# Kernel tuning notes

Measured on AMD Instinct MI355X. Metric: run time of the kernel, lower is better.

The kernel has to match this reference:

```python
import jax, jax.numpy as jnp
import numpy as np

SMPL_PARENTS = [-1, 0, 0, 0, 1, 2, 3, 4, 5, 6, 7, 8, 9, 9, 9, 12, 13, 14, 16, 17, 18, 19, 20, 21]
J = 24          # SMPL_NR_JOINTS
HID = 32        # hidden_dim
LSTM_H = HID * J  # 768

# Static skeleton adjacency incl. self loops (PyG GATConv add_self_loops=True).
# Edge (parent v -> child u): messages flow src=v to dst=u. adj[dst, src] = True.
_adj = np.eye(J, dtype=bool)
for u, v in enumerate(SMPL_PARENTS):
    if v >= 0:
        _adj[u, v] = True
ADJ = jnp.asarray(_adj)


def setup_inputs() -> dict:
    key = jax.random.key(0)
    ks = jax.random.split(key, 12)
    N, L = 128, 256
    s = lambda k, shp, scale: (jax.random.normal(k, shp, dtype=jnp.float32) * scale)
    return {
        "src": s(ks[0], (N, L, J * 3), 1.0),
        # pre: Linear(3 -> 32) + tanh
        "W_pre": s(ks[1], (3, HID), 0.3),
        "b_pre": s(ks[2], (HID,), 0.05),
        # GATConv(32 -> 32, heads=1): lin (no bias), att_src, att_dst, out bias
        "W_gat": s(ks[3], (HID, HID), 0.15),
        "att_src": s(ks[4], (HID,), 0.15),
        "att_dst": s(ks[5], (HID,), 0.15),
        "b_gat": s(ks[6], (HID,), 0.05),
        # LSTM(768 -> 768), gate order i, f, g, o (torch convention)
        "W_ih": s(ks[7], (4 * LSTM_H, LSTM_H), 0.02),
        "W_hh": s(ks[8], (4 * LSTM_H, LSTM_H), 0.02),
        "b_ih": s(ks[9], (4 * LSTM_H,), 0.02),
        "b_hh": s(ks[10], (4 * LSTM_H,), 0.02),
    }


def _gat_lstm(src, W_pre, b_pre, W_gat, att_src, att_dst, b_gat, W_ih, W_hh, b_ih, b_hh):
    N, L, D = src.shape
    A = D // J
    x = src.reshape(N * L, J, A)                       # [B, J, 3]
    x = jnp.tanh(x @ W_pre + b_pre)                    # pre: [B, J, H]

    # GATConv (heads=1, concat): vectorized over B copies of the static skeleton.
    xp = x @ W_gat                                     # [B, J, H]
    a_s = xp @ att_src                                 # [B, J] source term
    a_d = xp @ att_dst                                 # [B, J] dest term
    # e[b, i, j] = LeakyReLU(a_d[i] + a_s[j]) for edge j -> i (incl. self loops)
    e = jax.nn.leaky_relu(a_d[:, :, None] + a_s[:, None, :], negative_slope=0.2)
    e = jnp.where(ADJ[None, :, :], e, -jnp.inf)
    attn = jax.nn.softmax(e, axis=-1)                  # softmax over incoming edges
    g = jnp.einsum('bij,bjh->bih', attn, xp) + b_gat   # [B, J, H]

    X = g.reshape(N, L, J * HID)                       # from_graph_seq -> [N, L, 768]

    # LSTM (num_layers=1, batch_first), torch gate order i, f, g, o
    def step(carry, x_t):
        h, c = carry
        gates = x_t @ W_ih.T + b_ih + h @ W_hh.T + b_hh  # [N, 4*768]
        i_g, f_g, g_g, o_g = jnp.split(gates, 4, axis=-1)
        c = jax.nn.sigmoid(f_g) * c + jax.nn.sigmoid(i_g) * jnp.tanh(g_g)
        h = jax.nn.sigmoid(o_g) * jnp.tanh(c)
        return (h, c), h

    h0 = jnp.zeros((N, LSTM_H), dtype=X.dtype)
    (h_n, c_n), ys = jax.lax.scan(step, (h0, h0), X.transpose(1, 0, 2))
    output = ys.transpose(1, 0, 2)                     # [N, L, 768]
    return output, h_n[None], c_n[None]                # (out, (h_n, c_n)) like nn.LSTM


def reference(src, W_pre, b_pre, W_gat, att_src, att_dst, b_gat, W_ih, W_hh, b_ih, b_hh):
    return _gat_lstm(src, W_pre, b_pre, W_gat, att_src, att_dst, b_gat, W_ih, W_hh, b_ih, b_hh)
```

## Files before the change

### kernel.cpp

```cpp
#include <hip/hip_runtime.h>
#include <hip/hip_bf16.h>


#define NB 128
#define LSEQ 256
#define LH 768
#define BGR 32768
#define NWG 96
#define PWG 192

typedef __attribute__((ext_vector_type(8))) short short8;
typedef __attribute__((ext_vector_type(4))) float floatx4;
typedef __attribute__((ext_vector_type(4))) unsigned int uint4v;
typedef __attribute__((ext_vector_type(2))) unsigned int uint2v;

union frag16 { uint4v u; short8 s; };
union bfbits { __hip_bfloat16 h; unsigned short s; };
union uf2 { uint2v u; float f[2]; };

__device__ __forceinline__ float fsig(float x) {
    return __builtin_amdgcn_rcpf(1.f + __builtin_amdgcn_exp2f(-1.44269504f * x));
}
__device__ __forceinline__ float ftanhf(float x) {
    return 1.f - 2.f * __builtin_amdgcn_rcpf(1.f + __builtin_amdgcn_exp2f(2.88539008f * x));
}
__device__ __forceinline__ float fexpf(float x) {
    return __builtin_amdgcn_exp2f(1.44269504f * x);
}

__device__ __forceinline__ float bf16bits_to_f(unsigned short s) {
    unsigned u = ((unsigned)s) << 16;
    float f;
    __builtin_memcpy(&f, &u, 4);
    return f;
}

__device__ __forceinline__ void issue8(uint4v* b, const char* base) {
    asm volatile("global_load_dwordx4 %0, %1, off sc0 sc1"            : "=v"(b[0]) : "v"(base));
    asm volatile("global_load_dwordx4 %0, %1, off offset:64 sc0 sc1"  : "=v"(b[1]) : "v"(base));
    asm volatile("global_load_dwordx4 %0, %1, off offset:128 sc0 sc1" : "=v"(b[2]) : "v"(base));
    asm volatile("global_load_dwordx4 %0, %1, off offset:192 sc0 sc1" : "=v"(b[3]) : "v"(base));
    asm volatile("global_load_dwordx4 %0, %1, off offset:256 sc0 sc1" : "=v"(b[4]) : "v"(base));
    asm volatile("global_load_dwordx4 %0, %1, off offset:320 sc0 sc1" : "=v"(b[5]) : "v"(base));
    asm volatile("global_load_dwordx4 %0, %1, off offset:384 sc0 sc1" : "=v"(b[6]) : "v"(base));
    asm volatile("global_load_dwordx4 %0, %1, off offset:448 sc0 sc1" : "=v"(b[7]) : "v"(base));
}
__device__ __forceinline__ void issueG2(uint2v* g, const char* gb) {
    const char* gb2 = gb + 6144;
    asm volatile("global_load_dwordx2 %0, %1, off"             : "=v"(g[0]) : "v"(gb));
    asm volatile("global_load_dwordx2 %0, %1, off offset:3072" : "=v"(g[1]) : "v"(gb));
    asm volatile("global_load_dwordx2 %0, %1, off"             : "=v"(g[2]) : "v"(gb2));
    asm volatile("global_load_dwordx2 %0, %1, off offset:3072" : "=v"(g[3]) : "v"(gb2));
}
__device__ __forceinline__ void wait16g_touch(uint4v* b, uint2v* g) {
    asm volatile("s_waitcnt vmcnt(16)"
        : "+v"(b[0]), "+v"(b[1]), "+v"(b[2]), "+v"(b[3]),
          "+v"(b[4]), "+v"(b[5]), "+v"(b[6]), "+v"(b[7]),
          "+v"(g[0]), "+v"(g[1]), "+v"(g[2]), "+v"(g[3]) :: "memory");
}
__device__ __forceinline__ void wait8_touch(uint4v* b) {
    asm volatile("s_waitcnt vmcnt(8)"
        : "+v"(b[0]), "+v"(b[1]), "+v"(b[2]), "+v"(b[3]),
          "+v"(b[4]), "+v"(b[5]), "+v"(b[6]), "+v"(b[7]) :: "memory");
}
__device__ __forceinline__ void wait0_touch(uint4v* b) {
    asm volatile("s_waitcnt vmcnt(0)"
        : "+v"(b[0]), "+v"(b[1]), "+v"(b[2]), "+v"(b[3]),
          "+v"(b[4]), "+v"(b[5]), "+v"(b[6]), "+v"(b[7]) :: "memory");
}

__global__ __launch_bounds__(256) void convert_kernel(
    const float* W_pre, const float* b_pre, const float* W_gat,
    const float* att_src, const float* att_dst, const float* b_gat,
    const float* W_ih, const float* W_hh, const float* b_ih, const float* b_hh,
    __hip_bfloat16* __restrict__ WihC, __hip_bfloat16* __restrict__ WhhC,
    float* __restrict__ smallC)
{
    long i = (long)blockIdx.x * 256 + threadIdx.x;
    if (i < 2359296) { WihC[i] = __float2bfloat16(W_ih[i]); return; }
    i -= 2359296;
    if (i < 2359296) { WhhC[i] = __float2bfloat16(W_hh[i]); return; }
    i -= 2359296;
    if (i < 96)   { smallC[0 + i]    = W_pre[i];   return; }  i -= 96;
    if (i < 32)   { smallC[96 + i]   = b_pre[i];   return; }  i -= 32;
    if (i < 1024) { smallC[128 + i]  = W_gat[i];   return; }  i -= 1024;
    if (i < 32)   { smallC[1152 + i] = att_src[i]; return; }  i -= 32;
    if (i < 32)   { smallC[1184 + i] = att_dst[i]; return; }  i -= 32;
    if (i < 32)   { smallC[1216 + i] = b_gat[i];   return; }  i -= 32;
    if (i < 3072) { smallC[1248 + i] = b_ih[i];    return; }  i -= 3072;
    if (i < 3072) { smallC[4320 + i] = b_hh[i];    return; }
}

__global__ __launch_bounds__(256) void gat_pre_kernel(
    const float* __restrict__ src,
    const float* __restrict__ smallC,
    __hip_bfloat16* __restrict__ Xb)
{
    __shared__ float wpre[96];
    __shared__ float bpre[32];
    __shared__ float wgat[1024];
    __shared__ float asrc[32];
    __shared__ float adst[32];
    __shared__ float bgat[32];
    __shared__ float xl[8][72];
    __shared__ float hl[8][24][32];
    __shared__ float xpl[8][24][32];
    __shared__ float asl[8][24];
    __shared__ float adl[8][24];

    const int tid = threadIdx.x;
    for (int i = tid; i < 96; i += 256)   wpre[i] = smallC[i];
    for (int i = tid; i < 1024; i += 256) wgat[i] = smallC[128 + i];
    if (tid < 32) {
        bpre[tid] = smallC[96 + tid];
        asrc[tid] = smallC[1152 + tid];
        adst[tid] = smallC[1184 + tid];
        bgat[tid] = smallC[1216 + tid];
    }

    const int g = tid >> 5;
    const int k = tid & 31;
    const long gb = (long)blockIdx.x * 8 + g;

    for (int i = k; i < 72; i += 32)
        xl[g][i] = src[gb * 72 + i];
    __syncthreads();

    #pragma unroll
    for (int j = 0; j < 24; ++j) {
        float v = xl[g][j*3+0] * wpre[0*32+k]
                + xl[g][j*3+1] * wpre[1*32+k]
                + xl[g][j*3+2] * wpre[2*32+k] + bpre[k];
        hl[g][j][k] = ftanhf(v);
    }
    __syncthreads();

    #pragma unroll
    for (int j = 0; j < 24; ++j) {
        float v = 0.f;
        #pragma unroll
        for (int m = 0; m < 32; ++m) v += hl[g][j][m] * wgat[m*32 + k];
        xpl[g][j][k] = v;
    }
    __syncthreads();

    if (k < 24) {
        float vs = 0.f, vd = 0.f;
        #pragma unroll
        for (int m = 0; m < 32; ++m) {
            float x = xpl[g][k][m];
            vs += x * asrc[m];
            vd += x * adst[m];
        }
        asl[g][k] = vs;
        adl[g][k] = vd;
    }
    __syncthreads();

    const int par[24] = {-1,0,0,0,1,2,3,4,5,6,7,8,9,9,9,12,13,14,16,17,18,19,20,21};
    #pragma unroll
    for (int j = 0; j < 24; ++j) {
        int p = par[j];
        float o;
        if (p < 0) {
            o = xpl[g][j][k] + bgat[k];
        } else {
            float es = adl[g][j] + asl[g][j];
            float ep = adl[g][j] + asl[g][p];
            es = es > 0.f ? es : 0.2f * es;
            ep = ep > 0.f ? ep : 0.2f * ep;
            float mx = fmaxf(es, ep);
            float wse = fexpf(es - mx), wpe = fexpf(ep - mx);
            float inv = __builtin_amdgcn_rcpf(wse + wpe);
            o = (wse * xpl[g][j][k] + wpe * xpl[g][p][k]) * inv + bgat[k];
        }
        Xb[gb * 768 + j * 32 + k] = __float2bfloat16(o);
    }
}

__global__ __launch_bounds__(256) void gates_in_kernel(
    const __hip_bfloat16* __restrict__ Xb,
    const __hip_bfloat16* __restrict__ Wih,
    const float* __restrict__ smallC,
    float* __restrict__ Gf, __hip_bfloat16* __restrict__ Gb, int ginf)
{
    const int tid = threadIdx.x;
    const int w = tid >> 6, L = tid & 63;
    const int rh2 = w >> 1, ch2 = w & 1;
    const int q = L >> 4, col16 = L & 15;
    const int bid = blockIdx.x;
    const int g2 = bid >> 10;
    const int r2 = bid & 1023;
    const int R0 = (r2 >> 2) * 128;
    const int N0 = ((g2 << 2) | (r2 & 3)) * 128;

    const short8* ap[4];
    const short8* bp[4];
    #pragma unroll
    for (int i = 0; i < 4; ++i) {
        ap[i] = (const short8*)(Xb + (size_t)(R0 + 64*rh2 + 16*i + col16) * 768 + q*8);
        bp[i] = (const short8*)(Wih + (size_t)(N0 + 64*ch2 + 16*i + col16) * 768 + q*8);
    }

    floatx4 acc[4][4] = {};
    for (int kk = 0; kk < 24; ++kk) {
        short8 a[4], b[4];
        #pragma unroll
        for (int i = 0; i < 4; ++i) { a[i] = ap[i][kk*4]; b[i] = bp[i][kk*4]; }
        #pragma unroll
        for (int rt = 0; rt < 4; ++rt)
            #pragma unroll
            for (int bt = 0; bt < 4; ++bt)
                acc[rt][bt] = __builtin_amdgcn_mfma_f32_16x16x32_bf16(a[rt], b[bt], acc[rt][bt], 0, 0, 0);
    }

    #pragma unroll
    for (int bt = 0; bt < 4; ++bt) {
        int wrow = N0 + 64*ch2 + 16*bt + col16;
        float bias = smallC[1248 + wrow] + smallC[4320 + wrow];
        #pragma unroll
        for (int rt = 0; rt < 4; ++rt) {
            #pragma unroll
            for (int r = 0; r < 4; ++r) {
                int m_abs = R0 + 64*rh2 + 16*rt + q*4 + r;
                int mm = m_abs >> 8, tt = m_abs & 255;
                size_t idx = ((size_t)tt * 128 + mm) * 3072 + wrow;
                float v = acc[rt][bt][r] + bias;
                if (ginf) Gf[idx] = v;
                else      Gb[idx] = __float2bfloat16(v);
            }
        }
    }
}

__global__ __launch_bounds__(256) void lstm_persist_kernel(
    const void* __restrict__ Gin,
    const __hip_bfloat16* __restrict__ Whh,
    __hip_bfloat16* __restrict__ h0g,
    __hip_bfloat16* __restrict__ h1g,
    float* __restrict__ out,
    int* __restrict__ barU,
    int ginf)
{
    __shared__ short8 whhs[3072];
    __shared__ float gl[64 * 33];

    const int tid = threadIdx.x;
    const int w = tid >> 6;
    const int L = tid & 63;
    const int q = L >> 4;
    const int col16 = L & 15;
    const int cg = blockIdx.x % 96;
    const int rg = blockIdx.x / 96;

    for (int b = 0; b < 12; ++b) {
        int f = tid + 256 * b;
        int kk = f >> 7, c = (f >> 2) & 31, qq = f & 3;
        int wrow = 768 * (c >> 3) + cg * 8 + (c & 7);
        whhs[f] = *(const short8*)(Whh + (size_t)wrow * 768 + kk * 32 + qq * 8);
    }
    __syncthreads();

    const int m_loc = tid >> 2;
    const int u2b = (tid & 3) * 2;
    const int m_glob = rg * 64 + m_loc;
    float creg0 = 0.f, creg1 = 0.f;

    const float* Gf = (const float*)Gin;
    const __hip_bfloat16* Gb = (const __hip_bfloat16*)Gin;
    const size_t gcol = cg * 8 + u2b;

    int* myL1    = &barU[(rg * 16 + (cg & 7)) * 32];
    int* myL2    = &barU[(rg * 16 + 8) * 32];
    int* myEpoch = &barU[(rg * 16 + 9) * 32];

    uint2v gp[4] = {};
    if (ginf)
        issueG2(gp, (const char*)(Gf + (size_t)m_glob * 3072 + gcol));

    for (int t = 0; t < LSEQ; ++t) {
        const char* hr = (const char*)((t & 1) ? h1g : h0g);
        __hip_bfloat16* hw = (t & 1) ? h0g : h1g;

        floatx4 acc0 = {}, acc1 = {};
        uint4v bufA[8], bufB[8], bufC[8];
        const char* hbase = hr + (size_t)(((rg * 64 + 16 * w + col16) * 768) + q * 8) * 2;

        issue8(bufA, hbase);
        issue8(bufB, hbase + 512);
        issue8(bufC, hbase + 1024);

        wait16g_touch(bufA, gp);
        #pragma unroll
        for (int j = 0; j < 8; ++j) {
            frag16 fu; fu.u = bufA[j];
            short8 bv0 = whhs[j * 128 + (col16 * 4 + q)];
            short8 bv1 = whhs[j * 128 + ((16 + col16) * 4 + q)];
            acc0 = __builtin_amdgcn_mfma_f32_16x16x32_bf16(fu.s, bv0, acc0, 0, 0, 0);
            acc1 = __builtin_amdgcn_mfma_f32_16x16x32_bf16(fu.s, bv1, acc1, 0, 0, 0);
        }
        wait8_touch(bufB);
        #pragma unroll
        for (int j = 0; j < 8; ++j) {
            frag16 fu; fu.u = bufB[j];
            short8 bv0 = whhs[(8 + j) * 128 + (col16 * 4 + q)];
            short8 bv1 = whhs[(8 + j) * 128 + ((16 + col16) * 4 + q)];
            acc0 = __builtin_amdgcn_mfma_f32_16x16x32_bf16(fu.s, bv0, acc0, 0, 0, 0);
            acc1 = __builtin_amdgcn_mfma_f32_16x16x32_bf16(fu.s, bv1, acc1, 0, 0, 0);
        }
        wait0_touch(bufC);
        #pragma unroll
        for (int j = 0; j < 8; ++j) {
            frag16 fu; fu.u = bufC[j];
            short8 bv0 = whhs[(16 + j) * 128 + (col16 * 4 + q)];
            short8 bv1 = whhs[(16 + j) * 128 + ((16 + col16) * 4 + q)];
            acc0 = __builtin_amdgcn_mfma_f32_16x16x32_bf16(fu.s, bv0, acc0, 0, 0, 0);
            acc1 = __builtin_amdgcn_mfma_f32_16x16x32_bf16(fu.s, bv1, acc1, 0, 0, 0);
        }

        #pragma unroll
        for (int r = 0; r < 4; ++r) {
            int mr = 16 * w + q * 4 + r;
            gl[mr * 33 + col16] = acc0[r];
            gl[mr * 33 + 16 + col16] = acc1[r];
        }
        __syncthreads();

        float gI0, gI1, gF0, gF1, gG0, gG1, gO0, gO1;
        if (ginf) {
            uf2 uI, uF, uG, uO;
            uI.u = gp[0]; uF.u = gp[1]; uG.u = gp[2]; uO.u = gp[3];
            gI0 = uI.f[0]; gI1 = uI.f[1]; gF0 = uF.f[0]; gF1 = uF.f[1];
            gG0 = uG.f[0]; gG1 = uG.f[1]; gO0 = uO.f[0]; gO1 = uO.f[1];
        } else {
            const size_t grow = ((size_t)t * 128 + m_glob) * 3072 + gcol;
            unsigned vi = *(const unsigned*)(Gb + grow);
            unsigned vf = *(const unsigned*)(Gb + grow + 768);
            unsigned vg = *(const unsigned*)(Gb + grow + 1536);
            unsigned vo = *(const unsigned*)(Gb + grow + 2304);
            gI0 = bf16bits_to_f(vi & 0xFFFF); gI1 = bf16bits_to_f(vi >> 16);
            gF0 = bf16bits_to_f(vf & 0xFFFF); gF1 = bf16bits_to_f(vf >> 16);
            gG0 = bf16bits_to_f(vg & 0xFFFF); gG1 = bf16bits_to_f(vg >> 16);
            gO0 = bf16bits_to_f(vo & 0xFFFF); gO1 = bf16bits_to_f(vo >> 16);
        }

        float ig0 = gI0 + gl[m_loc * 33 + 0  + u2b];
        float fg0 = gF0 + gl[m_loc * 33 + 8  + u2b];
        float gg0 = gG0 + gl[m_loc * 33 + 16 + u2b];
        float og0 = gO0 + gl[m_loc * 33 + 24 + u2b];
        float ig1 = gI1 + gl[m_loc * 33 + 0  + u2b + 1];
        float fg1 = gF1 + gl[m_loc * 33 + 8  + u2b + 1];
        float gg1 = gG1 + gl[m_loc * 33 + 16 + u2b + 1];
        float og1 = gO1 + gl[m_loc * 33 + 24 + u2b + 1];

        float si0 = fsig(ig0), sf0 = fsig(fg0), so0 = fsig(og0);
        float cn0 = sf0 * creg0 + si0 * ftanhf(gg0);
        float hv0 = so0 * ftanhf(cn0);
        creg0 = cn0;
        float si1 = fsig(ig1), sf1 = fsig(fg1), so1 = fsig(og1);
        float cn1 = sf1 * creg1 + si1 * ftanhf(gg1);
        float hv1 = so1 * ftanhf(cn1);
        creg1 = cn1;

        bfbits b0, b1;
        b0.h = __float2bfloat16(hv0);
        b1.h = __float2bfloat16(hv1);
        unsigned hpack = (unsigned)b0.s | ((unsigned)b1.s << 16);
        char* ha = (char*)hw + (size_t)(m_glob * 768 + cg * 8 + u2b) * 2;
        float2 ov; ov.x = hv0; ov.y = hv1;
        float* oa = out + ((size_t)m_glob * 256 + t) * 768 + cg * 8 + u2b;

        if (t < LSEQ - 1) {
            asm volatile("global_store_dword %0, %1, off sc0 sc1" :: "v"(ha), "v"(hpack) : "memory");
            asm volatile("global_store_dwordx2 %0, %1, off" :: "v"(oa), "v"(ov) : "memory");
            if (ginf)
                issueG2(gp, (const char*)(Gf + ((size_t)(t + 1) * 128 + m_glob) * 3072 + gcol));
            asm volatile("s_waitcnt vmcnt(5)" ::: "memory");
            __builtin_amdgcn_s_barrier();
            if (tid == 0) {
                int prev = __hip_atomic_fetch_add(myL1, 1,
                                                  __ATOMIC_RELAXED, __HIP_MEMORY_SCOPE_AGENT);
                bool rel = false;
                if (prev == 12 * (t + 1) - 1) {
                    int pr = __hip_atomic_fetch_add(myL2, 1,
                                                    __ATOMIC_RELAXED, __HIP_MEMORY_SCOPE_AGENT);
                    if (pr == 8 * (t + 1) - 1) {
                        __hip_atomic_store(myEpoch, t + 1,
                                           __ATOMIC_RELAXED, __HIP_MEMORY_SCOPE_AGENT);
                        rel = true;
                    }
                }
                if (!rel) {
                    while (__hip_atomic_load(myEpoch, __ATOMIC_RELAXED,
                                             __HIP_MEMORY_SCOPE_AGENT) < t + 1)
                        __builtin_amdgcn_s_sleep(1);
                }
            }
            __builtin_amdgcn_s_barrier();
        } else {
            asm volatile("global_store_dwordx2 %0, %1, off" :: "v"(oa), "v"(ov) : "memory");
            const size_t base = (size_t)NB * LSEQ * LH;
            const size_t ci = (size_t)m_glob * 768 + cg * 8 + u2b;
            float2 hv; hv.x = hv0; hv.y = hv1;
            float2 cv; cv.x = cn0; cv.y = cn1;
            *(float2*)(out + base + ci) = hv;
            *(float2*)(out + base + (size_t)NB * LH + ci) = cv;
        }
    }
}

__global__ __launch_bounds__(256) void lstm_step_kernel(
    const __hip_bfloat16* __restrict__ Xb,
    const __hip_bfloat16* __restrict__ Wih,
    const __hip_bfloat16* __restrict__ Whh,
    const float* __restrict__ smallC,
    float* __restrict__ cst,
    const __hip_bfloat16* __restrict__ hr,
    __hip_bfloat16* __restrict__ hw,
    float* __restrict__ out,
    int t)
{
    __shared__ float gls[128 * 33];
    const int tid = threadIdx.x;
    const int w = tid >> 6;
    const int L = tid & 63;
    const int rh = w >> 1;
    const int ct = w & 1;
    const int q = L >> 4;
    const int col16 = L & 15;
    const int c_local = 16 * ct + col16;
    const int gate = c_local >> 3;
    const int uu = c_local & 7;
    const int u = 8 * blockIdx.x + uu;
    const int wrow = 768 * gate + u;

    const short8* bp_i = (const short8*)(Wih + (long)wrow * 768 + q * 8);
    const short8* bp_h = (const short8*)(Whh + (long)wrow * 768 + q * 8);
    const short8* ap_x[4];
    const short8* ap_h[4];
    #pragma unroll
    for (int rt = 0; rt < 4; ++rt) {
        int m = 64 * rh + 16 * rt + col16;
        ap_x[rt] = (const short8*)(Xb + ((long)m * LSEQ + t) * 768 + q * 8);
        ap_h[rt] = (const short8*)(hr + (long)m * 768 + q * 8);
    }
    floatx4 acc[4] = {};
    for (int kk = 0; kk < 768; kk += 32) {
        short8 bv = bp_i[kk >> 3];
        #pragma unroll
        for (int rt = 0; rt < 4; ++rt)
            acc[rt] = __builtin_amdgcn_mfma_f32_16x16x32_bf16(ap_x[rt][kk >> 3], bv, acc[rt], 0, 0, 0);
    }
    for (int kk = 0; kk < 768; kk += 32) {
        short8 bv = bp_h[kk >> 3];
        #pragma unroll
        for (int rt = 0; rt < 4; ++rt)
            acc[rt] = __builtin_amdgcn_mfma_f32_16x16x32_bf16(ap_h[rt][kk >> 3], bv, acc[rt], 0, 0, 0);
    }
    float bias = smallC[1248 + wrow] + smallC[4320 + wrow];
    #pragma unroll
    for (int rt = 0; rt < 4; ++rt)
        #pragma unroll
        for (int r = 0; r < 4; ++r) {
            int m = 64 * rh + 16 * rt + q * 4 + r;
            gls[m * 33 + c_local] = acc[rt][r] + bias;
        }
    __syncthreads();
    for (int item = tid; item < 1024; item += 256) {
        int m = item >> 3;
        int u2l = item & 7;
        float ig = gls[m * 33 + 0  + u2l];
        float fg = gls[m * 33 + 8  + u2l];
        float gg = gls[m * 33 + 16 + u2l];
        float og = gls[m * 33 + 24 + u2l];
        int u2 = 8 * blockIdx.x + u2l;
        int ci = m * 768 + u2;
        float co = cst[ci];
        float si = 1.f / (1.f + expf(-ig));
        float sf = 1.f / (1.f + expf(-fg));
        float so = 1.f / (1.f + expf(-og));
        float cn = sf * co + si * tanhf(gg);
        float h = so * tanhf(cn);
        cst[ci] = cn;
        hw[ci] = __float2bfloat16(h);
        out[((long)m * LSEQ + t) * 768 + u2] = h;
    }
}

__global__ __launch_bounds__(256) void finalize_kernel(
    const __hip_bfloat16* __restrict__ hfin,
    const float* __restrict__ cst,
    float* __restrict__ out)
{
    int i = blockIdx.x * 256 + threadIdx.x;
    const long base = (long)NB * LSEQ * LH;
    out[base + i] = __bfloat162float(hfin[i]);
    out[base + NB * LH + i] = cst[i];
}

extern "C" void kernel_launch(void* const* d_in, const int* in_sizes, int n_in,
                              void* d_out, int out_size, void* d_ws, size_t ws_size,
                              hipStream_t stream) {
    const float* src     = (const float*)d_in[0];
    const float* W_pre   = (const float*)d_in[1];
    const float* b_pre   = (const float*)d_in[2];
    const float* W_gat   = (const float*)d_in[3];
    const float* att_src = (const float*)d_in[4];
    const float* att_dst = (const float*)d_in[5];
    const float* b_gat   = (const float*)d_in[6];
    const float* W_ih    = (const float*)d_in[7];
    const float* W_hh    = (const float*)d_in[8];
    const float* b_ih    = (const float*)d_in[9];
    const float* b_hh    = (const float*)d_in[10];

    float* out = (float*)d_out;
    char* ws = (char*)d_ws;

    __hip_bfloat16* Xb     = (__hip_bfloat16*)(ws);
    __hip_bfloat16* WihC   = (__hip_bfloat16*)(ws + 50331648);
    __hip_bfloat16* WhhC   = (__hip_bfloat16*)(ws + 55050240);
    float*          cs     = (float*)         (ws + 59768832);
    __hip_bfloat16* h0     = (__hip_bfloat16*)(ws + 60162048);
    __hip_bfloat16* h1     = (__hip_bfloat16*)(ws + 60358656);
    float*          smallC = (float*)         (ws + 60555264);
    void*           Gin    = (void*)          (ws + 60596224);

    const size_t base_need = 60596224;
    const size_t need_f32  = base_need + (size_t)BGR * 3072 * 4;
    const size_t need_b16  = base_need + (size_t)BGR * 3072 * 2;
    const int use_persist  = (ws_size >= need_b16);
    const int ginf         = (ws_size >= need_f32);

    hipMemsetAsync(h0, 0, NB * LH * sizeof(__hip_bfloat16), stream);

    const long conv_total = 2359296L * 2 + 7392;
    convert_kernel<<<(int)((conv_total + 255) / 256), 256, 0, stream>>>(
        W_pre, b_pre, W_gat, att_src, att_dst, b_gat,
        W_ih, W_hh, b_ih, b_hh, WihC, WhhC, smallC);

    gat_pre_kernel<<<BGR / 8, 256, 0, stream>>>(src, smallC, Xb);

    if (use_persist) {
        hipMemsetAsync(cs, 0, 327680, stream);
        gates_in_kernel<<<6144, 256, 0, stream>>>(Xb, WihC, smallC,
                                                  (float*)Gin, (__hip_bfloat16*)Gin, ginf);
        lstm_persist_kernel<<<PWG, 256, 0, stream>>>(Gin, WhhC, h0, h1, out,
                                                     (int*)cs, ginf);
    } else {
        hipMemsetAsync(cs, 0, NB * LH * sizeof(float), stream);
        __hip_bfloat16* hp[2] = {h0, h1};
        for (int t = 0; t < LSEQ; ++t) {
            lstm_step_kernel<<<NWG, 256, 0, stream>>>(Xb, WihC, WhhC, smallC,
                                                      cs, hp[t & 1], hp[(t + 1) & 1],
                                                      out, t);
        }
        finalize_kernel<<<NB * LH / 256, 256, 0, stream>>>(h0, cs, out);
    }
}
```

Baseline: 2.416 ms.

## Fuse input-gate GEMM producers with persistent LSTM consumers via per-timestep flags

Merges the input-projection GEMM into the persistent LSTM launch. Extra producer workgroups compute the per-timestep gate inputs and publish completion flags, and consumer workgroups spin on the flag for step t+2 before continuing. This overlaps the large input GEMM with the serial recurrence instead of running them back to back. It removes the bf16 fallback path, assumes the producer and consumer workgroups are co-resident, and adds coherent store and load traffic plus flag polling.

```diff
diff --git a/kernel.cpp b/kernel.cpp
--- a/kernel.cpp
+++ b/kernel.cpp
@@ -8,6 +8,7 @@
 #define BGR 32768
 #define NWG 96
 #define PWG 192
+#define NPROD 256
 
 typedef __attribute__((ext_vector_type(8))) short short8;
 typedef __attribute__((ext_vector_type(4))) float floatx4;
@@ -26,13 +27,6 @@
 }
 __device__ __forceinline__ float fexpf(float x) {
     return __builtin_amdgcn_exp2f(1.44269504f * x);
-}
-
-__device__ __forceinline__ float bf16bits_to_f(unsigned short s) {
-    unsigned u = ((unsigned)s) << 16;
-    float f;
-    __builtin_memcpy(&f, &u, 4);
-    return f;
 }
 
 __device__ __forceinline__ void issue8(uint4v* b, const char* base) {
@@ -45,12 +39,12 @@
     asm volatile("global_load_dwordx4 %0, %1, off offset:384 sc0 sc1" : "=v"(b[6]) : "v"(base));
     asm volatile("global_load_dwordx4 %0, %1, off offset:448 sc0 sc1" : "=v"(b[7]) : "v"(base));
 }
-__device__ __forceinline__ void issueG2(uint2v* g, const char* gb) {
+__device__ __forceinline__ void issueG2c(uint2v* g, const char* gb) {
     const char* gb2 = gb + 6144;
-    asm volatile("global_load_dwordx2 %0, %1, off"             : "=v"(g[0]) : "v"(gb));
-    asm volatile("global_load_dwordx2 %0, %1, off offset:3072" : "=v"(g[1]) : "v"(gb));
-    asm volatile("global_load_dwordx2 %0, %1, off"             : "=v"(g[2]) : "v"(gb2));
-    asm volatile("global_load_dwordx2 %0, %1, off offset:3072" : "=v"(g[3]) : "v"(gb2));
+    asm volatile("global_load_dwordx2 %0, %1, off sc0 sc1"             : "=v"(g[0]) : "v"(gb));
+    asm volatile("global_load_dwordx2 %0, %1, off offset:3072 sc0 sc1" : "=v"(g[1]) : "v"(gb));
+    asm volatile("global_load_dwordx2 %0, %1, off sc0 sc1"             : "=v"(g[2]) : "v"(gb2));
+    asm volatile("global_load_dwordx2 %0, %1, off offset:3072 sc0 sc1" : "=v"(g[3]) : "v"(gb2));
 }
 __device__ __forceinline__ void wait16g_touch(uint4v* b, uint2v* g) {
     asm volatile("s_waitcnt vmcnt(16)"
@@ -178,74 +172,82 @@
     }
 }
 
-__global__ __launch_bounds__(256) void gates_in_kernel(
+__global__ __launch_bounds__(256) void lstm_fused_kernel(
+    float* __restrict__ G,
+    const __hip_bfloat16* __restrict__ Whh,
     const __hip_bfloat16* __restrict__ Xb,
     const __hip_bfloat16* __restrict__ Wih,
     const float* __restrict__ smallC,
-    float* __restrict__ Gf, __hip_bfloat16* __restrict__ Gb, int ginf)
-{
-    const int tid = threadIdx.x;
-    const int w = tid >> 6, L = tid & 63;
-    const int rh2 = w >> 1, ch2 = w & 1;
-    const int q = L >> 4, col16 = L & 15;
-    const int bid = blockIdx.x;
-    const int g2 = bid >> 10;
-    const int r2 = bid & 1023;
-    const int R0 = (r2 >> 2) * 128;
-    const int N0 = ((g2 << 2) | (r2 & 3)) * 128;
-
-    const short8* ap[4];
-    const short8* bp[4];
-    #pragma unroll
-    for (int i = 0; i < 4; ++i) {
-        ap[i] = (const short8*)(Xb + (size_t)(R0 + 64*rh2 + 16*i + col16) * 768 + q*8);
-        bp[i] = (const short8*)(Wih + (size_t)(N0 + 64*ch2 + 16*i + col16) * 768 + q*8);
-    }
-
-    floatx4 acc[4][4] = {};
-    for (int kk = 0; kk < 24; ++kk) {
-        short8 a[4], b[4];
-        #pragma unroll
-        for (int i = 0; i < 4; ++i) { a[i] = ap[i][kk*4]; b[i] = bp[i][kk*4]; }
-        #pragma unroll
-        for (int rt = 0; rt < 4; ++rt)
-            #pragma unroll
-            for (int bt = 0; bt < 4; ++bt)
-                acc[rt][bt] = __builtin_amdgcn_mfma_f32_16x16x32_bf16(a[rt], b[bt], acc[rt][bt], 0, 0, 0);
-    }
-
-    #pragma unroll
-    for (int bt = 0; bt < 4; ++bt) {
-        int wrow = N0 + 64*ch2 + 16*bt + col16;
-        float bias = smallC[1248 + wrow] + smallC[4320 + wrow];
-        #pragma unroll
-        for (int rt = 0; rt < 4; ++rt) {
-            #pragma unroll
-            for (int r = 0; r < 4; ++r) {
-                int m_abs = R0 + 64*rh2 + 16*rt + q*4 + r;
-                int mm = m_abs >> 8, tt = m_abs & 255;
-                size_t idx = ((size_t)tt * 128 + mm) * 3072 + wrow;
-                float v = acc[rt][bt][r] + bias;
-                if (ginf) Gf[idx] = v;
-                else      Gb[idx] = __float2bfloat16(v);
-            }
-        }
-    }
-}
-
-__global__ __launch_bounds__(256) void lstm_persist_kernel(
-    const void* __restrict__ Gin,
-    const __hip_bfloat16* __restrict__ Whh,
     __hip_bfloat16* __restrict__ h0g,
     __hip_bfloat16* __restrict__ h1g,
     float* __restrict__ out,
-    int* __restrict__ barU,
-    int ginf)
+    int* __restrict__ barU)
 {
     __shared__ short8 whhs[3072];
     __shared__ float gl[64 * 33];
 
     const int tid = threadIdx.x;
+
+    if (blockIdx.x >= PWG) {
+        const int pid = blockIdx.x - PWG;
+        const int w2 = tid >> 6, L2v = tid & 63;
+        const int rh2 = w2 >> 1, ch2 = w2 & 1;
+        const int q2 = L2v >> 4, c16 = L2v & 15;
+
+        for (int idx = pid; idx < 6144; idx += NPROD) {
+            const int t = idx / 24;
+            const int nb = idx - t * 24;
+            const int N0 = nb * 128;
+
+            const short8* ap[4];
+            const short8* bp[4];
+            #pragma unroll
+            for (int i = 0; i < 4; ++i) {
+                int n = 64 * rh2 + 16 * i + c16;
+                ap[i] = (const short8*)(Xb + ((size_t)n * 256 + t) * 768 + q2 * 8);
+                bp[i] = (const short8*)(Wih + (size_t)(N0 + 64 * ch2 + 16 * i + c16) * 768 + q2 * 8);
+            }
+
+            floatx4 acc[4][4] = {};
+            for (int kk = 0; kk < 24; ++kk) {
+                short8 a[4], b[4];
+                #pragma unroll
+                for (int i = 0; i < 4; ++i) { a[i] = ap[i][kk * 4]; b[i] = bp[i][kk * 4]; }
+                #pragma unroll
+                for (int rt = 0; rt < 4; ++rt)
+                    #pragma unroll
+                    for (int bt = 0; bt < 4; ++bt)
+                        acc[rt][bt] = __builtin_amdgcn_mfma_f32_16x16x32_bf16(a[rt], b[bt], acc[rt][bt], 0, 0, 0);
+            }
+
+            #pragma unroll
+            for (int bt = 0; bt < 4; ++bt) {
+                int wrow = N0 + 64 * ch2 + 16 * bt + c16;
+                float bias = smallC[1248 + wrow] + smallC[4320 + wrow];
+                #pragma unroll
+                for (int rt = 0; rt < 4; ++rt) {
+                    #pragma unroll
+                    for (int r = 0; r < 4; ++r) {
+                        int n = 64 * rh2 + 16 * rt + q2 * 4 + r;
+                        float v = acc[rt][bt][r] + bias;
+                        float* ga = G + ((size_t)t * 128 + n) * 3072 + wrow;
+                        asm volatile("global_store_dword %0, %1, off sc0 sc1" :: "v"(ga), "v"(v) : "memory");
+                    }
+                }
+            }
+            asm volatile("s_waitcnt vmcnt(0)" ::: "memory");
+            __syncthreads();
+            if (tid == 0) {
+                int prev = __hip_atomic_fetch_add(&barU[(64 + t) * 32], 1,
+                                                  __ATOMIC_RELAXED, __HIP_MEMORY_SCOPE_AGENT);
+                if (prev == 23)
+                    __hip_atomic_store(&barU[(320 + t) * 32], 1,
+                                       __ATOMIC_RELAXED, __HIP_MEMORY_SCOPE_AGENT);
+            }
+        }
+        return;
+    }
+
     const int w = tid >> 6;
     const int L = tid & 63;
     const int q = L >> 4;
@@ -265,18 +267,24 @@
     const int u2b = (tid & 3) * 2;
     const int m_glob = rg * 64 + m_loc;
     float creg0 = 0.f, creg1 = 0.f;
-
-    const float* Gf = (const float*)Gin;
-    const __hip_bfloat16* Gb = (const __hip_bfloat16*)Gin;
     const size_t gcol = cg * 8 + u2b;
 
     int* myL1    = &barU[(rg * 16 + (cg & 7)) * 32];
     int* myL2    = &barU[(rg * 16 + 8) * 32];
     int* myEpoch = &barU[(rg * 16 + 9) * 32];
 
+    if (tid == 0) {
+        while (__hip_atomic_load(&barU[(320 + 0) * 32], __ATOMIC_RELAXED,
+                                 __HIP_MEMORY_SCOPE_AGENT) == 0)
+            __builtin_amdgcn_s_sleep(1);
+        while (__hip_atomic_load(&barU[(320 + 1) * 32], __ATOMIC_RELAXED,
+                                 __HIP_MEMORY_SCOPE_AGENT) == 0)
+            __builtin_amdgcn_s_sleep(1);
+    }
+    __builtin_amdgcn_s_barrier();
+
     uint2v gp[4] = {};
-    if (ginf)
-        issueG2(gp, (const char*)(Gf + (size_t)m_glob * 3072 + gcol));
+    issueG2c(gp, (const char*)(G + (size_t)m_glob * 3072 + gcol));
 
     for (int t = 0; t < LSEQ; ++t) {
         const char* hr = (const char*)((t & 1) ? h1g : h0g);
@@ -326,32 +334,17 @@
         }
         __syncthreads();
 
-        float gI0, gI1, gF0, gF1, gG0, gG1, gO0, gO1;
-        if (ginf) {
-            uf2 uI, uF, uG, uO;
-            uI.u = gp[0]; uF.u = gp[1]; uG.u = gp[2]; uO.u = gp[3];
-            gI0 = uI.f[0]; gI1 = uI.f[1]; gF0 = uF.f[0]; gF1 = uF.f[1];
-            gG0 = uG.f[0]; gG1 = uG.f[1]; gO0 = uO.f[0]; gO1 = uO.f[1];
-        } else {
-            const size_t grow = ((size_t)t * 128 + m_glob) * 3072 + gcol;
-            unsigned vi = *(const unsigned*)(Gb + grow);
-            unsigned vf = *(const unsigned*)(Gb + grow + 768);
-            unsigned vg = *(const unsigned*)(Gb + grow + 1536);
-            unsigned vo = *(const unsigned*)(Gb + grow + 2304);
-            gI0 = bf16bits_to_f(vi & 0xFFFF); gI1 = bf16bits_to_f(vi >> 16);
-            gF0 = bf16bits_to_f(vf & 0xFFFF); gF1 = bf16bits_to_f(vf >> 16);
-            gG0 = bf16bits_to_f(vg & 0xFFFF); gG1 = bf16bits_to_f(vg >> 16);
-            gO0 = bf16bits_to_f(vo & 0xFFFF); gO1 = bf16bits_to_f(vo >> 16);
-        }
-
-        float ig0 = gI0 + gl[m_loc * 33 + 0  + u2b];
-        float fg0 = gF0 + gl[m_loc * 33 + 8  + u2b];
-        float gg0 = gG0 + gl[m_loc * 33 + 16 + u2b];
-        float og0 = gO0 + gl[m_loc * 33 + 24 + u2b];
-        float ig1 = gI1 + gl[m_loc * 33 + 0  + u2b + 1];
-        float fg1 = gF1 + gl[m_loc * 33 + 8  + u2b + 1];
-        float gg1 = gG1 + gl[m_loc * 33 + 16 + u2b + 1];
-        float og1 = gO1 + gl[m_loc * 33 + 24 + u2b + 1];
+        uf2 uI, uF, uG, uO;
+        uI.u = gp[0]; uF.u = gp[1]; uG.u = gp[2]; uO.u = gp[3];
+
+        float ig0 = uI.f[0] + gl[m_loc * 33 + 0  + u2b];
+        float fg0 = uF.f[0] + gl[m_loc * 33 + 8  + u2b];
+        float gg0 = uG.f[0] + gl[m_loc * 33 + 16 + u2b];
+        float og0 = uO.f[0] + gl[m_loc * 33 + 24 + u2b];
+        float ig1 = uI.f[1] + gl[m_loc * 33 + 0  + u2b + 1];
+        float fg1 = uF.f[1] + gl[m_loc * 33 + 8  + u2b + 1];
+        float gg1 = uG.f[1] + gl[m_loc * 33 + 16 + u2b + 1];
+        float og1 = uO.f[1] + gl[m_loc * 33 + 24 + u2b + 1];
 
         float si0 = fsig(ig0), sf0 = fsig(fg0), so0 = fsig(og0);
         float cn0 = sf0 * creg0 + si0 * ftanhf(gg0);
@@ -373,8 +366,7 @@
         if (t < LSEQ - 1) {
             asm volatile("global_store_dword %0, %1, off sc0 sc1" :: "v"(ha), "v"(hpack) : "memory");
             asm volatile("global_store_dwordx2 %0, %1, off" :: "v"(oa), "v"(ov) : "memory");
-            if (ginf)
-                issueG2(gp, (const char*)(Gf + ((size_t)(t + 1) * 128 + m_glob) * 3072 + gcol));
+            issueG2c(gp, (const char*)(G + ((size_t)(t + 1) * 128 + m_glob) * 3072 + gcol));
             asm volatile("s_waitcnt vmcnt(5)" ::: "memory");
             __builtin_amdgcn_s_barrier();
             if (tid == 0) {
@@ -393,6 +385,11 @@
                 if (!rel) {
                     while (__hip_atomic_load(myEpoch, __ATOMIC_RELAXED,
                                              __HIP_MEMORY_SCOPE_AGENT) < t + 1)
+                        __builtin_amdgcn_s_sleep(1);
+                }
+                if (t + 2 < LSEQ) {
+                    while (__hip_atomic_load(&barU[(320 + t + 2) * 32], __ATOMIC_RELAXED,
+                                             __HIP_MEMORY_SCOPE_AGENT) == 0)
                         __builtin_amdgcn_s_sleep(1);
                 }
             }
@@ -523,13 +520,10 @@
     __hip_bfloat16* h0     = (__hip_bfloat16*)(ws + 60162048);
     __hip_bfloat16* h1     = (__hip_bfloat16*)(ws + 60358656);
     float*          smallC = (float*)         (ws + 60555264);
-    void*           Gin    = (void*)          (ws + 60596224);
-
-    const size_t base_need = 60596224;
-    const size_t need_f32  = base_need + (size_t)BGR * 3072 * 4;
-    const size_t need_b16  = base_need + (size_t)BGR * 3072 * 2;
-    const int use_persist  = (ws_size >= need_b16);
-    const int ginf         = (ws_size >= need_f32);
+    float*          Gin    = (float*)         (ws + 60596224);
+
+    const size_t need_f32 = 60596224 + (size_t)BGR * 3072 * 4;
+    const int use_persist = (ws_size >= need_f32);
 
     hipMemsetAsync(h0, 0, NB * LH * sizeof(__hip_bfloat16), stream);
 
@@ -542,10 +536,8 @@
 
     if (use_persist) {
         hipMemsetAsync(cs, 0, 327680, stream);
-        gates_in_kernel<<<6144, 256, 0, stream>>>(Xb, WihC, smallC,
-                                                  (float*)Gin, (__hip_bfloat16*)Gin, ginf);
-        lstm_persist_kernel<<<PWG, 256, 0, stream>>>(Gin, WhhC, h0, h1, out,
-                                                     (int*)cs, ginf);
+        lstm_fused_kernel<<<PWG + NPROD, 256, 0, stream>>>(
+            Gin, WhhC, Xb, WihC, smallC, h0, h1, out, (int*)cs);
     } else {
         hipMemsetAsync(cs, 0, NB * LH * sizeof(float), stream);
         __hip_bfloat16* hp[2] = {h0, h1};
```

New measurement: 8.098 ms. 3.35x slower.
